# Optimization experiments

Hardware: AMD Instinct MI355X
Metric: run time of the kernel (lower is better)

The kernel has to match this reference:

```python
import jax, jax.numpy as jnp
import numpy as np

EPS = 1e-6

def quantize_weights(W):
    # absmean ternary quantization: gamma = mean(|W|) + eps; round(|W|/gamma) clamped to <=1, with sign
    gamma = jnp.mean(jnp.abs(W)) + EPS
    W_scaled = W / gamma
    return jnp.sign(W_scaled) * jnp.minimum(jnp.round(jnp.abs(W_scaled)), 1.0)

def setup_inputs() -> dict:
    key = jax.random.key(0)
    kx, kw = jax.random.split(key)
    x = jax.random.normal(kx, (4, 4096, 2048), dtype=jnp.float32)
    weight = jax.random.normal(kw, (2048, 2048), dtype=jnp.float32)  # [out_features, in_features]
    return {"x": x, "weight": weight}

def reference(x, weight):
    x_sign = jnp.sign(x)                      # sign activation: {-1, 0, +1}
    Wq = quantize_weights(weight)             # ternary weights {-1, 0, +1}
    # F.linear(x, W) = x @ W.T -> (..., out_features)
    return jnp.einsum('bsi,oi->bso', x_sign, Wq)
```

## Files before the change

kernel.cpp:

```cpp
#include <hip/hip_runtime.h>
#include <hip/hip_bf16.h>

typedef __attribute__((ext_vector_type(4))) int i32x4;
typedef unsigned char u8;


__global__ void kabs_partial(const float* __restrict__ W, double* __restrict__ part, int n) {
    __shared__ double sd[256];
    const int tid = threadIdx.x;
    double s = 0.0;
    for (int i = blockIdx.x * blockDim.x + tid; i < n; i += gridDim.x * blockDim.x)
        s += (double)fabsf(W[i]);
    sd[tid] = s;
    __syncthreads();
    for (int off = 128; off > 0; off >>= 1) {
        if (tid < off) sd[tid] += sd[tid + off];
        __syncthreads();
    }
    if (tid == 0) part[blockIdx.x] = sd[0];
}

__global__ void kgamma(const double* __restrict__ part, float* __restrict__ gout, int nelem) {
    __shared__ double sd[256];
    const int tid = threadIdx.x;
    double s = part[tid] + part[tid + 256] + part[tid + 512] + part[tid + 768];
    sd[tid] = s;
    __syncthreads();
    for (int off = 128; off > 0; off >>= 1) {
        if (tid < off) sd[tid] += sd[tid + off];
        __syncthreads();
    }
    if (tid == 0) gout[0] = (float)(sd[0] / (double)nelem) + 1e-6f;
}


__device__ __forceinline__ unsigned int qw_b(float w, float g) {
    float t = fabsf(w) / g;
    unsigned int u = __float_as_uint(w);
    return (rintf(t) >= 1.0f) ? ((u >> 31) ? 0xFFu : 0x01u) : 0u;
}

__global__ void kquant_w(const float4* __restrict__ W4, unsigned int* __restrict__ Wq,
                         const float* __restrict__ gptr, int n4) {
    int i = blockIdx.x * blockDim.x + threadIdx.x;
    if (i >= n4) return;
    const float g = *gptr;
    float4 w = W4[i];
    Wq[i] = qw_b(w.x, g) | (qw_b(w.y, g) << 8) | (qw_b(w.z, g) << 16) | (qw_b(w.w, g) << 24);
}

__device__ __forceinline__ unsigned int sgn_b(float a) {
    unsigned int u = __float_as_uint(a);
    return (u & 0x7FFFFFFFu) ? ((u >> 31) ? 0xFFu : 0x01u) : 0u;
}
__device__ __forceinline__ unsigned int sgn4(float4 v) {
    return sgn_b(v.x) | (sgn_b(v.y) << 8) | (sgn_b(v.z) << 16) | (sgn_b(v.w) << 24);
}

__global__ void kquant_x(const float4* __restrict__ X4, uint4* __restrict__ Xq, size_t n16) {
    size_t i = (size_t)blockIdx.x * blockDim.x + threadIdx.x;
    if (i >= n16) return;
    uint4 o;
    o.x = sgn4(X4[4 * i]);
    o.y = sgn4(X4[4 * i + 1]);
    o.z = sgn4(X4[4 * i + 2]);
    o.w = sgn4(X4[4 * i + 3]);
    Xq[i] = o;
}


#define STAGE_HALF(SRC, DST, BASE_ROW, KB)                                                  \
    {                                                                                       \
        _Pragma("unroll")                                                                   \
        for (int l = 0; l < 2; ++l) {                                                       \
            const int r_ = l * 64 + srow;                                                   \
            const u8* g_ = (SRC) + (size_t)((BASE_ROW) + r_) * K + (KB) +                   \
                           (sec ^ ((r_ & 7) << 4));                                         \
            __builtin_amdgcn_global_load_lds(                                               \
                (const __attribute__((address_space(1))) unsigned int*)g_,                  \
                (__attribute__((address_space(3))) unsigned int*)&(DST)[r_][sec], 16, 0, 0);\
        }                                                                                   \
    }

#define BARRIER do { asm volatile("" ::: "memory"); __builtin_amdgcn_s_barrier(); \
                     asm volatile("" ::: "memory"); } while (0)
#define LGKM0   do { asm volatile("s_waitcnt lgkmcnt(0)" ::: "memory"); \
                     __builtin_amdgcn_sched_barrier(0); } while (0)
#define VMC6    asm volatile("s_waitcnt vmcnt(6)" ::: "memory")

#define DS_READ_A(BUF, m, dst)                                                              \
    {                                                                                       \
        const int ra = wm * 64 + ((m) & 3) * 16 + lr;                                       \
        _Pragma("unroll")                                                                   \
        for (int ks = 0; ks < 2; ++ks)                                                      \
            dst[ks] = *(const i32x4*)&As[BUF][(m) >> 2][ra][(ks * 64 + lk16) ^ ((ra & 7) << 4)]; \
    }

#define DS_READ_B(BUF)                                                                      \
    {                                                                                       \
        _Pragma("unroll")                                                                   \
        for (int n = 0; n < 4; ++n) {                                                       \
            const int rb = (wn & 1) * 64 + n * 16 + lr;                                     \
            _Pragma("unroll")                                                               \
            for (int ks = 0; ks < 2; ++ks)                                                  \
                bv[n][ks] = *(const i32x4*)&Bs[BUF][wn >> 1][rb][(ks * 64 + lk16) ^ ((rb & 7) << 4)]; \
        }                                                                                   \
    }

#define MFMA_PH(mb, AV)                                                                     \
    do {                                                                                    \
        __builtin_amdgcn_s_setprio(1);                                                      \
        _Pragma("unroll")                                                                   \
        for (int mi = 0; mi < 2; ++mi)                                                      \
            _Pragma("unroll")                                                               \
            for (int n = 0; n < 4; ++n)                                                     \
                _Pragma("unroll")                                                           \
                for (int ks = 0; ks < 2; ++ks)                                              \
                    acc[(mb) + mi][n] = __builtin_amdgcn_mfma_i32_16x16x64_i8(              \
                        AV[mi][ks], bv[n][ks], acc[(mb) + mi][n], 0, 0, 0);                 \
        __builtin_amdgcn_s_setprio(0);                                                      \
    } while (0)

__global__ __launch_bounds__(512, 2) void kgemm(const u8* __restrict__ A,
                                                const u8* __restrict__ B,
                                                float* __restrict__ C,
                                                int M, int N, int K) {
    __shared__ u8 As[2][2][128][128];
    __shared__ u8 Bs[2][2][128][128];

    const int tid = threadIdx.x;
    const int lane = tid & 63;
    const int wid = tid >> 6;
    const int wm = wid >> 2;
    const int wn = wid & 3;

    int bid = blockIdx.x;
    const int nwg = gridDim.x;
    if ((nwg & 7) == 0) bid = (bid & 7) * (nwg >> 3) + (bid >> 3);
    const int nbn = N >> 8;
    const int bm = bid / nbn, bn = bid % nbn;
    const int row0 = bm << 8, col0 = bn << 8;

    const int lr = lane & 15;
    const int lk16 = (lane >> 4) * 16;

    const int srow = tid >> 3;
    const int sec  = (tid & 7) * 16;

    i32x4 acc[8][4] = {};
    const int NT = K >> 7;

    STAGE_HALF(B, Bs[0][0], col0, 0);
    STAGE_HALF(B, Bs[0][1], col0 + 128, 0);
    STAGE_HALF(A, As[0][0], row0, 0);
    STAGE_HALF(A, As[0][1], row0 + 128, 0);
    STAGE_HALF(B, Bs[1][0], col0, 128);
    STAGE_HALF(B, Bs[1][1], col0 + 128, 128);
    STAGE_HALF(A, As[1][0], row0, 128);
    VMC6;
    BARRIER;

    i32x4 bv[4][2], av0[2][2], av1[2][2];
    DS_READ_B(0);
    DS_READ_A(0, 0, av0[0]); DS_READ_A(0, 1, av0[1]);

    for (int t = 0; t < NT; t += 2) {
        const int kb1 = (t + 1) << 7;
        const int kb2 = (t + 2 < NT ? t + 2 : NT - 1) << 7;
        const int kb3 = (t + 3 < NT ? t + 3 : NT - 1) << 7;

        STAGE_HALF(A, As[1][1], row0 + 128, kb1);
        BARRIER; LGKM0;
        MFMA_PH(0, av0);
        DS_READ_A(0, 2, av1[0]); DS_READ_A(0, 3, av1[1]);
        STAGE_HALF(B, Bs[0][0], col0, kb2);
        BARRIER; LGKM0;
        MFMA_PH(2, av1);
        DS_READ_A(0, 4, av0[0]); DS_READ_A(0, 5, av0[1]);
        STAGE_HALF(B, Bs[0][1], col0 + 128, kb2);
        BARRIER; LGKM0;
        MFMA_PH(4, av0);
        DS_READ_A(0, 6, av1[0]); DS_READ_A(0, 7, av1[1]);
        STAGE_HALF(A, As[0][0], row0, kb2);
        VMC6;
        BARRIER; LGKM0;
        MFMA_PH(6, av1);
        DS_READ_B(1);
        DS_READ_A(1, 0, av0[0]); DS_READ_A(1, 1, av0[1]);
        STAGE_HALF(A, As[0][1], row0 + 128, kb2);
        BARRIER; LGKM0;
        MFMA_PH(0, av0);
        DS_READ_A(1, 2, av1[0]); DS_READ_A(1, 3, av1[1]);
        STAGE_HALF(B, Bs[1][0], col0, kb3);
        BARRIER; LGKM0;
        MFMA_PH(2, av1);
        DS_READ_A(1, 4, av0[0]); DS_READ_A(1, 5, av0[1]);
        STAGE_HALF(B, Bs[1][1], col0 + 128, kb3);
        BARRIER; LGKM0;
        MFMA_PH(4, av0);
        DS_READ_A(1, 6, av1[0]); DS_READ_A(1, 7, av1[1]);
        STAGE_HALF(A, As[1][0], row0, kb3);
        VMC6;
        BARRIER; LGKM0;
        MFMA_PH(6, av1);
        DS_READ_B(0);
        DS_READ_A(0, 0, av0[0]); DS_READ_A(0, 1, av0[1]);
    }
    asm volatile("s_waitcnt vmcnt(0) lgkmcnt(0)" ::: "memory");

#pragma unroll
    for (int m = 0; m < 8; ++m) {
        const int grow = row0 + (m >> 2) * 128 + wm * 64 + (m & 3) * 16 + (lane >> 4) * 4;
#pragma unroll
        for (int n = 0; n < 4; ++n) {
            float* cp = C + (size_t)grow * N + col0 + wn * 64 + n * 16 + (lane & 15);
#pragma unroll
            for (int r = 0; r < 4; ++r)
                cp[(size_t)r * N] = (float)acc[m][n][r];
        }
    }
}


__global__ void knaive(const float* __restrict__ X, const float* __restrict__ W,
                       const float* __restrict__ gptr, float* __restrict__ out,
                       int N, int K) {
    size_t idx = (size_t)blockIdx.x * blockDim.x + threadIdx.x;
    const int m = (int)(idx / N), n = (int)(idx % N);
    const float g = *gptr;
    const float* xr = X + (size_t)m * K;
    const float* wrow = W + (size_t)n * K;
    float acc = 0.f;
    for (int k = 0; k < K; ++k) {
        float xv = xr[k];
        float xs = (xv > 0.f) ? 1.f : ((xv < 0.f) ? -1.f : 0.f);
        float w = wrow[k];
        float wq = (rintf(fabsf(w) / g) >= 1.f) ? ((w < 0.f) ? -1.f : 1.f) : 0.f;
        acc += xs * wq;
    }
    out[idx] = acc;
}


extern "C" void kernel_launch(void* const* d_in, const int* in_sizes, int n_in,
                              void* d_out, int out_size, void* d_ws, size_t ws_size,
                              hipStream_t stream) {
    const float* x = (const float*)d_in[0];
    const float* W = (const float*)d_in[1];
    float* out = (float*)d_out;

    const int K = 2048;
    const int N = in_sizes[1] / K;
    const int M = in_sizes[0] / K;
    const int nW = in_sizes[1];

    char* ws = (char*)d_ws;
    double* partials = (double*)ws;
    float* gamma = (float*)(ws + 8192);
    u8* wq = (u8*)(ws + 16384);
    u8* xq = (u8*)(ws + 16384 + (size_t)N * K);
    const size_t need = 16384 + (size_t)N * K + (size_t)M * K;

    kabs_partial<<<1024, 256, 0, stream>>>(W, partials, nW);
    kgamma<<<1, 256, 0, stream>>>(partials, gamma, nW);

    if (ws_size >= need && (M % 256) == 0 && (N % 256) == 0 && (K % 256) == 0) {
        kquant_w<<<nW / (256 * 4), 256, 0, stream>>>((const float4*)W, (unsigned int*)wq,
                                                     gamma, nW / 4);
        const size_t n16 = (size_t)M * K / 16;
        kquant_x<<<(unsigned)((n16 + 255) / 256), 256, 0, stream>>>(
            (const float4*)x, (uint4*)xq, n16);
        kgemm<<<(M / 256) * (N / 256), 512, 0, stream>>>(xq, wq, out, M, N, K);
    } else {
        knaive<<<(unsigned)((size_t)M * N / 256), 256, 0, stream>>>(x, W, gamma, out, N, K);
    }
}
```

Baseline: 125.0 us.

## Halve barrier count per K-tile by issuing four-row MFMA phases

Reworks the GEMM main loop so each phase reads four A fragments and issues 32 MFMAs instead of two fragments and 16 MFMAs. This cuts the barriers per 128-wide K tile from four to two. Global-to-LDS staging is regrouped to two half-tiles per phase, with a matching vmcnt(4) wait and a reordered prologue. The final LDS prefetch in each iteration is now guarded so it is skipped on the last iteration. In exchange, more A-fragment registers are held and each barrier phase has less slack for load latency, which could hurt occupancy or overlap.

```diff
diff --git a/kernel.cpp b/kernel.cpp
--- a/kernel.cpp
+++ b/kernel.cpp
@@ -86,14 +86,19 @@
                      asm volatile("" ::: "memory"); } while (0)
 #define LGKM0   do { asm volatile("s_waitcnt lgkmcnt(0)" ::: "memory"); \
                      __builtin_amdgcn_sched_barrier(0); } while (0)
-#define VMC6    asm volatile("s_waitcnt vmcnt(6)" ::: "memory")
-
-#define DS_READ_A(BUF, m, dst)                                                              \
+#define VMC4    asm volatile("s_waitcnt vmcnt(4)" ::: "memory")
+
+#define DS_READ_A4(BUF, mb, dst)                                                            \
     {                                                                                       \
-        const int ra = wm * 64 + ((m) & 3) * 16 + lr;                                       \
-        _Pragma("unroll")                                                                   \
-        for (int ks = 0; ks < 2; ++ks)                                                      \
-            dst[ks] = *(const i32x4*)&As[BUF][(m) >> 2][ra][(ks * 64 + lk16) ^ ((ra & 7) << 4)]; \
+        _Pragma("unroll")                                                                   \
+        for (int mi = 0; mi < 4; ++mi) {                                                    \
+            const int m_ = (mb) + mi;                                                       \
+            const int ra = wm * 64 + (m_ & 3) * 16 + lr;                                    \
+            _Pragma("unroll")                                                               \
+            for (int ks = 0; ks < 2; ++ks)                                                  \
+                dst[mi][ks] = *(const i32x4*)&As[BUF][m_ >> 2][ra]                          \
+                                  [(ks * 64 + lk16) ^ ((ra & 7) << 4)];                     \
+        }                                                                                   \
     }
 
 #define DS_READ_B(BUF)                                                                      \
@@ -103,15 +108,16 @@
             const int rb = (wn & 1) * 64 + n * 16 + lr;                                     \
             _Pragma("unroll")                                                               \
             for (int ks = 0; ks < 2; ++ks)                                                  \
-                bv[n][ks] = *(const i32x4*)&Bs[BUF][wn >> 1][rb][(ks * 64 + lk16) ^ ((rb & 7) << 4)]; \
+                bv[n][ks] = *(const i32x4*)&Bs[BUF][wn >> 1][rb]                            \
+                                [(ks * 64 + lk16) ^ ((rb & 7) << 4)];                       \
         }                                                                                   \
     }
 
-#define MFMA_PH(mb, AV)                                                                     \
+#define MFMA4(mb, AV)                                                                       \
     do {                                                                                    \
         __builtin_amdgcn_s_setprio(1);                                                      \
         _Pragma("unroll")                                                                   \
-        for (int mi = 0; mi < 2; ++mi)                                                      \
+        for (int mi = 0; mi < 4; ++mi)                                                      \
             _Pragma("unroll")                                                               \
             for (int n = 0; n < 4; ++n)                                                     \
                 _Pragma("unroll")                                                           \
@@ -154,15 +160,14 @@
     STAGE_HALF(B, Bs[0][1], col0 + 128, 0);
     STAGE_HALF(A, As[0][0], row0, 0);
     STAGE_HALF(A, As[0][1], row0 + 128, 0);
+    STAGE_HALF(A, As[1][0], row0, 128);
     STAGE_HALF(B, Bs[1][0], col0, 128);
-    STAGE_HALF(B, Bs[1][1], col0 + 128, 128);
-    STAGE_HALF(A, As[1][0], row0, 128);
-    VMC6;
+    VMC4;
     BARRIER;
 
-    i32x4 bv[4][2], av0[2][2], av1[2][2];
+    i32x4 bv[4][2], av0[4][2], av1[4][2];
     DS_READ_B(0);
-    DS_READ_A(0, 0, av0[0]); DS_READ_A(0, 1, av0[1]);
+    DS_READ_A4(0, 0, av0);
 
     for (int t = 0; t < NT; t += 2) {
         const int kb1 = (t + 1) << 7;
@@ -170,41 +175,31 @@
         const int kb3 = (t + 3 < NT ? t + 3 : NT - 1) << 7;
 
         STAGE_HALF(A, As[1][1], row0 + 128, kb1);
-        BARRIER; LGKM0;
-        MFMA_PH(0, av0);
-        DS_READ_A(0, 2, av1[0]); DS_READ_A(0, 3, av1[1]);
+        STAGE_HALF(B, Bs[1][1], col0 + 128, kb1);
+        BARRIER; LGKM0;
+        MFMA4(0, av0);
+        DS_READ_A4(0, 4, av1);
+        STAGE_HALF(A, As[0][0], row0, kb2);
         STAGE_HALF(B, Bs[0][0], col0, kb2);
-        BARRIER; LGKM0;
-        MFMA_PH(2, av1);
-        DS_READ_A(0, 4, av0[0]); DS_READ_A(0, 5, av0[1]);
+        VMC4;
+        BARRIER; LGKM0;
+        MFMA4(4, av1);
+        DS_READ_B(1);
+        DS_READ_A4(1, 0, av0);
         STAGE_HALF(B, Bs[0][1], col0 + 128, kb2);
-        BARRIER; LGKM0;
-        MFMA_PH(4, av0);
-        DS_READ_A(0, 6, av1[0]); DS_READ_A(0, 7, av1[1]);
-        STAGE_HALF(A, As[0][0], row0, kb2);
-        VMC6;
-        BARRIER; LGKM0;
-        MFMA_PH(6, av1);
-        DS_READ_B(1);
-        DS_READ_A(1, 0, av0[0]); DS_READ_A(1, 1, av0[1]);
         STAGE_HALF(A, As[0][1], row0 + 128, kb2);
         BARRIER; LGKM0;
-        MFMA_PH(0, av0);
-        DS_READ_A(1, 2, av1[0]); DS_READ_A(1, 3, av1[1]);
+        MFMA4(0, av0);
+        DS_READ_A4(1, 4, av1);
+        STAGE_HALF(A, As[1][0], row0, kb3);
         STAGE_HALF(B, Bs[1][0], col0, kb3);
-        BARRIER; LGKM0;
-        MFMA_PH(2, av1);
-        DS_READ_A(1, 4, av0[0]); DS_READ_A(1, 5, av0[1]);
-        STAGE_HALF(B, Bs[1][1], col0 + 128, kb3);
-        BARRIER; LGKM0;
-        MFMA_PH(4, av0);
-        DS_READ_A(1, 6, av1[0]); DS_READ_A(1, 7, av1[1]);
-        STAGE_HALF(A, As[1][0], row0, kb3);
-        VMC6;
-        BARRIER; LGKM0;
-        MFMA_PH(6, av1);
-        DS_READ_B(0);
-        DS_READ_A(0, 0, av0[0]); DS_READ_A(0, 1, av0[1]);
+        VMC4;
+        BARRIER; LGKM0;
+        MFMA4(4, av1);
+        if (t + 2 < NT) {
+            DS_READ_B(0);
+            DS_READ_A4(0, 0, av0);
+        }
     }
     asm volatile("s_waitcnt vmcnt(0) lgkmcnt(0)" ::: "memory");
 
```

Measured after the change: 126.1 us. About the same (+0.9%).
